# Performance work log

Hardware: AMD Instinct MI355X
Metric: run time of the kernel (lower is better)

Reference implementation:

```python
import jax, jax.numpy as jnp
import numpy as np

MAX_GRAD = 200.0


@jax.custom_vjp
def sqrt_bound_derivative(x):
    return jnp.sqrt(x)


def _sqrt_bd_fwd(x):
    return jnp.sqrt(x), x


def _sqrt_bd_bwd(x, g):
    # derivative of sqrt clipped to MAX_GRAD: 0.5/sqrt(x) <= MAX_GRAD  <=>  x >= 1/(4*MAX_GRAD^2)
    x_clipped = jnp.maximum(x, 1.0 / (4.0 * MAX_GRAD * MAX_GRAD))
    return (g * 0.5 / jnp.sqrt(x_clipped),)


sqrt_bound_derivative.defvjp(_sqrt_bd_fwd, _sqrt_bd_bwd)


def linear_scan(a, x, h0):
    # h_t = a_t * h_{t-1} + x_t, diagonal recurrence over axis=1 (time).
    # Parallel form via associative scan on pairs (a, b): combine -> (a1*a2, a2*b1 + b2).
    def combine(c1, c2):
        a1, b1 = c1
        a2, b2 = c2
        return a1 * a2, a2 * b1 + b2

    a_cum, h = jax.lax.associative_scan(combine, (a, x), axis=1)
    # fold in initial state: h_t += (prod_{u<=t} a_u) * h0
    h = h + a_cum * h0[:, None, :]
    return h, h[:, -1]


def setup_inputs() -> dict:
    key = jax.random.key(0)
    ks = jax.random.split(key, 8)
    B, S, D_IN, D_HID, D_OUT = 8, 4096, 512, 1024, 512
    R_MIN, R_MAX = 0.9, 0.999

    x = jax.random.normal(ks[0], (B, S, D_IN), dtype=jnp.float32)
    h0 = jnp.zeros((B, D_HID), dtype=jnp.float32)

    # stable_init: a_logit = logit(U(r_min, r_max)) so that a = sigmoid(a_logit) in [r_min, r_max]
    u = jax.random.uniform(ks[1], (D_HID,), minval=R_MIN, maxval=R_MAX)
    a_logit = jnp.log(u) - jnp.log1p(-u)

    def dense_init(k, d_in, d_out):
        scale = 1.0 / np.sqrt(d_in)
        return jax.random.uniform(k, (d_in, d_out), minval=-scale, maxval=scale).astype(jnp.float32)

    W_dx = dense_init(ks[2], D_IN, D_OUT)
    b_dx = jnp.zeros((D_OUT,), dtype=jnp.float32)
    W_in = dense_init(ks[3], D_IN, D_HID)
    b_in = jnp.zeros((D_HID,), dtype=jnp.float32)
    W_out = dense_init(ks[4], D_HID, D_OUT)
    b_out = jnp.zeros((D_OUT,), dtype=jnp.float32)

    return {"x": x, "h0": h0, "a_logit": a_logit,
            "W_dx": W_dx, "b_dx": b_dx,
            "W_in": W_in, "b_in": b_in,
            "W_out": W_out, "b_out": b_out}


def reference(x, h0, a_logit, W_dx, b_dx, W_in, b_in, W_out, b_out):
    a = jax.nn.sigmoid(a_logit)                      # (d_hidden,)
    dx = jnp.einsum('bsi,io->bso', x, W_dx) + b_dx   # skip projection (b, s, d_out)
    u = jnp.einsum('bsi,ih->bsh', x, W_in) + b_in    # input projection (b, s, d_hidden)
    u = sqrt_bound_derivative(1.0 - a * a) * u       # input_norm gating
    a_b = jnp.broadcast_to(a, u.shape)
    h, h_last = linear_scan(a_b, u, h0)              # diagonal linear recurrence
    out = (dx + jnp.einsum('bsh,ho->bso', h, W_out) + b_out) / 2.0
    return out, h_last
```

## Files before the change

### kernel.cpp

```cpp
#include <hip/hip_runtime.h>

#define B_    8
#define S_    4096
#define DIN   512
#define DHID  1024
#define DOUT  512
#define M_    (B_*S_)
#define NCAT  (DHID + DOUT)
#define CH2   32
#define NCH2  (S_/CH2)

typedef __bf16 bf16x8 __attribute__((ext_vector_type(8)));
typedef float  floatx4 __attribute__((ext_vector_type(4)));

__device__ __forceinline__ unsigned short f2bf(float f) {
  unsigned u = __builtin_bit_cast(unsigned, f);
  u = (u + 0x7FFFu + ((u >> 16) & 1u)) >> 16;
  return (unsigned short)u;
}
__device__ __forceinline__ float bf2f(unsigned short h) {
  unsigned u = ((unsigned)h) << 16;
  return __builtin_bit_cast(float, u);
}

__device__ __forceinline__ void gl_lds16(const unsigned short* g, unsigned short* l) {
  __builtin_amdgcn_global_load_lds((const __attribute__((address_space(1))) void*)g,
                                   (__attribute__((address_space(3))) void*)l, 16, 0, 0);
}

__global__ void prep_as(const float* __restrict__ logit, float* __restrict__ a_s) {
  int d = blockIdx.x * 256 + threadIdx.x;
  if (d < DHID) {
    float a = 1.f / (1.f + expf(-logit[d]));
    a_s[d] = a;
    a_s[DHID + d] = sqrtf(fmaxf(1.f - a * a, 0.f));
  }
}

__global__ void prep_x(const float* __restrict__ x, unsigned short* __restrict__ xb) {
  size_t i = (size_t)blockIdx.x * 256 + threadIdx.x;
  const float4* p = (const float4*)x;
  float4 v0 = p[i * 2];
  float4 v1 = p[i * 2 + 1];
  uint4 o;
  o.x = (unsigned)f2bf(v0.x) | ((unsigned)f2bf(v0.y) << 16);
  o.y = (unsigned)f2bf(v0.z) | ((unsigned)f2bf(v0.w) << 16);
  o.z = (unsigned)f2bf(v1.x) | ((unsigned)f2bf(v1.y) << 16);
  o.w = (unsigned)f2bf(v1.z) | ((unsigned)f2bf(v1.w) << 16);
  *(uint4*)&xb[i * 8] = o;
}

__global__ void prep_wcat(const float* __restrict__ Win, const float* __restrict__ Wdx,
                          unsigned short* __restrict__ wcat) {
  int idx = blockIdx.x * 256 + threadIdx.x;
  int n = idx >> 9, k = idx & 511;
  float v = (n < DHID) ? Win[(size_t)k * DHID + n] : Wdx[(size_t)k * DOUT + (n - DHID)];
  wcat[idx] = f2bf(v);
}

__global__ void prep_wout(const float* __restrict__ Wout, unsigned short* __restrict__ wt) {
  int idx = blockIdx.x * 256 + threadIdx.x;
  int n = idx >> 10, k = idx & 1023;
  wt[idx] = f2bf(Wout[(size_t)k * DOUT + n]);
}

template <int K, int MODE, int NB>
__global__ __launch_bounds__(256, 4) void gemm_bt(
    const unsigned short* __restrict__ A,
    const unsigned short* __restrict__ Bt,
    const float* __restrict__ a_s,
    const float* __restrict__ bias0,
    const float* __restrict__ bias1,
    unsigned short* __restrict__ u_out,
    unsigned short* __restrict__ dx_buf,
    float* __restrict__ out)
{
  __shared__ __align__(16) unsigned char smem[32768];
  unsigned short* lA = (unsigned short*)smem;
  unsigned short* lB = (unsigned short*)(smem + 16384);
  float* stg = (float*)smem;

  const int tid = threadIdx.x;
  const int flat = blockIdx.y * gridDim.x + blockIdx.x;
  const int xcd = flat & 7;
  const int j = flat >> 3;
  const int n0 = (j % NB) * 128;
  const int m0 = ((j / NB) * 8 + xcd) * 128;

  const int wid = tid >> 6, lane = tid & 63;
  const int wm = (wid >> 1) * 64, wn = (wid & 1) * 64;
  const int r16 = lane & 15, quad = lane >> 4;
  const int sw = r16 & 7;

  const int rsub = lane >> 3;
  const int gcol = ((lane & 7) ^ rsub) << 3;

  const unsigned short* Abase = A + (size_t)(m0 + (wid << 5) + rsub) * K + gcol;
  const unsigned short* Bbase = Bt + (size_t)(n0 + (wid << 5) + rsub) * K + gcol;
  unsigned short* lAw = lA + (wid << 5) * 64;
  unsigned short* lBw = lB + (wid << 5) * 64;

  floatx4 acc[4][4] = {};

  for (int k0 = 0; k0 < K; k0 += 64) {
#pragma unroll
    for (int i = 0; i < 4; ++i) {
      gl_lds16(Abase + (size_t)(i * 8) * K + k0, lAw + i * 8 * 64);
      gl_lds16(Bbase + (size_t)(i * 8) * K + k0, lBw + i * 8 * 64);
    }
    __syncthreads();
#pragma unroll
    for (int ks = 0; ks < 2; ++ks) {
      bf16x8 af[4], bfr[4];
#pragma unroll
      for (int i = 0; i < 4; ++i)
        af[i] = *(const bf16x8*)&lA[(wm + i * 16 + r16) * 64 + ((((ks << 2) | quad) ^ sw) << 3)];
#pragma unroll
      for (int j2 = 0; j2 < 4; ++j2)
        bfr[j2] = *(const bf16x8*)&lB[(wn + j2 * 16 + r16) * 64 + ((((ks << 2) | quad) ^ sw) << 3)];
#pragma unroll
      for (int i = 0; i < 4; ++i)
#pragma unroll
        for (int j2 = 0; j2 < 4; ++j2)
          acc[i][j2] = __builtin_amdgcn_mfma_f32_16x16x32_bf16(af[i], bfr[j2], acc[i][j2], 0, 0, 0);
    }
    __syncthreads();
  }

  const int row = tid >> 3;
  const int seg = tid & 7;
#pragma unroll
  for (int p = 0; p < 4; ++p) {
    __syncthreads();
    if ((wid >> 1) == (p >> 1)) {
      const int i0 = (p & 1) * 2;
#pragma unroll
      for (int ii = 0; ii < 2; ++ii) {
        const int i = i0 + ii;
        const int srow = i * 16 + quad * 4 - (p & 1) * 32;
#pragma unroll
        for (int j2 = 0; j2 < 4; ++j2) {
          const int scol = wn + j2 * 16 + r16;
#pragma unroll
          for (int r = 0; r < 4; ++r)
            stg[(srow + r) * 132 + scol] = acc[i][j2][r];
        }
      }
    }
    __syncthreads();
    const int gm = m0 + p * 32 + row;
    const int col0 = n0 + seg * 16;
    if (MODE == 0) {
      union { unsigned short s[16]; uint4 q[2]; } ub;
      if (n0 < DHID) {
#pragma unroll
        for (int u = 0; u < 4; ++u) {
          float4 v  = *(const float4*)&stg[row * 132 + seg * 16 + u * 4];
          float4 bi = *(const float4*)&bias0[col0 + u * 4];
          float4 sc = *(const float4*)&a_s[DHID + col0 + u * 4];
          ub.s[u * 4 + 0] = f2bf((v.x + bi.x) * sc.x);
          ub.s[u * 4 + 1] = f2bf((v.y + bi.y) * sc.y);
          ub.s[u * 4 + 2] = f2bf((v.z + bi.z) * sc.z);
          ub.s[u * 4 + 3] = f2bf((v.w + bi.w) * sc.w);
        }
        *(uint4*)&u_out[(size_t)gm * DHID + col0]     = ub.q[0];
        *(uint4*)&u_out[(size_t)gm * DHID + col0 + 8] = ub.q[1];
      } else {
        const int c2 = col0 - DHID;
#pragma unroll
        for (int u = 0; u < 4; ++u) {
          float4 v  = *(const float4*)&stg[row * 132 + seg * 16 + u * 4];
          float4 bd = *(const float4*)&bias1[c2 + u * 4];
          ub.s[u * 4 + 0] = f2bf(v.x + bd.x);
          ub.s[u * 4 + 1] = f2bf(v.y + bd.y);
          ub.s[u * 4 + 2] = f2bf(v.z + bd.z);
          ub.s[u * 4 + 3] = f2bf(v.w + bd.w);
        }
        *(uint4*)&dx_buf[(size_t)gm * DOUT + c2]     = ub.q[0];
        *(uint4*)&dx_buf[(size_t)gm * DOUT + c2 + 8] = ub.q[1];
      }
    } else {
#pragma unroll
      for (int u = 0; u < 4; ++u) {
        float4 v  = *(const float4*)&stg[row * 132 + seg * 16 + u * 4];
        float4 bo = *(const float4*)&bias0[col0 + u * 4];
        ushort4 dv = *(const ushort4*)&dx_buf[(size_t)gm * DOUT + col0 + u * 4];
        float4 o;
        o.x = (v.x + bo.x + bf2f(dv.x)) * 0.5f;
        o.y = (v.y + bo.y + bf2f(dv.y)) * 0.5f;
        o.z = (v.z + bo.z + bf2f(dv.z)) * 0.5f;
        o.w = (v.w + bo.w + bf2f(dv.w)) * 0.5f;
        *(float4*)&out[(size_t)gm * DOUT + col0 + u * 4] = o;
      }
    }
  }
}

__global__ __launch_bounds__(256) void scan1(const unsigned short* __restrict__ u,
                                             const float* __restrict__ a_s,
                                             float* __restrict__ carry) {
  int idx = blockIdx.x * 256 + threadIdx.x;
  int d8 = (idx & 127) * 8;
  int c  = (idx >> 7) & (NCH2 - 1);
  int b  = idx >> 14;
  float4 a0 = *(const float4*)&a_s[d8];
  float4 a1 = *(const float4*)&a_s[d8 + 4];
  float h0_ = 0.f, h1 = 0.f, h2 = 0.f, h3 = 0.f, h4 = 0.f, h5 = 0.f, h6 = 0.f, h7 = 0.f;
  const unsigned short* up = u + ((size_t)(b * S_ + c * CH2)) * DHID + d8;
#pragma unroll 4
  for (int t = 0; t < CH2; ++t) {
    ushort4 q0 = *(const ushort4*)up;
    ushort4 q1 = *(const ushort4*)(up + 4);
    h0_ = fmaf(a0.x, h0_, bf2f(q0.x)); h1 = fmaf(a0.y, h1, bf2f(q0.y));
    h2  = fmaf(a0.z, h2,  bf2f(q0.z)); h3 = fmaf(a0.w, h3, bf2f(q0.w));
    h4  = fmaf(a1.x, h4,  bf2f(q1.x)); h5 = fmaf(a1.y, h5, bf2f(q1.y));
    h6  = fmaf(a1.z, h6,  bf2f(q1.z)); h7 = fmaf(a1.w, h7, bf2f(q1.w));
    up += DHID;
  }
  float* cp = &carry[((size_t)(b * NCH2 + c)) * DHID + d8];
  float4 o0 = {h0_, h1, h2, h3}, o1 = {h4, h5, h6, h7};
  *(float4*)cp = o0;
  *(float4*)(cp + 4) = o1;
}

__global__ __launch_bounds__(256) void scan_mid(const float* __restrict__ a_s,
                                                const float* __restrict__ h0,
                                                float* __restrict__ carry,
                                                float* __restrict__ h_last) {
  int idx = blockIdx.x * 256 + threadIdx.x;
  int d = idx & (DHID - 1);
  int b = idx >> 10;
  float a = a_s[d];
  float aL = a;
#pragma unroll
  for (int q = 0; q < 5; ++q) aL *= aL;
  float st = h0[(size_t)b * DHID + d];
  float* p = &carry[(size_t)b * NCH2 * DHID + d];
  for (int cg = 0; cg < NCH2; cg += 8) {
    float loc[8];
#pragma unroll
    for (int j = 0; j < 8; ++j) loc[j] = p[(size_t)j * DHID];
#pragma unroll
    for (int j = 0; j < 8; ++j) {
      p[(size_t)j * DHID] = st;
      st = fmaf(aL, st, loc[j]);
    }
    p += (size_t)8 * DHID;
  }
  h_last[(size_t)b * DHID + d] = st;
}

__global__ __launch_bounds__(256) void scan2(unsigned short* __restrict__ u,
                                             const float* __restrict__ a_s,
                                             const float* __restrict__ carry) {
  int idx = blockIdx.x * 256 + threadIdx.x;
  int d8 = (idx & 127) * 8;
  int c  = (idx >> 7) & (NCH2 - 1);
  int b  = idx >> 14;
  float4 a0 = *(const float4*)&a_s[d8];
  float4 a1 = *(const float4*)&a_s[d8 + 4];
  const float* cp = &carry[((size_t)(b * NCH2 + c)) * DHID + d8];
  float4 e0 = *(const float4*)cp;
  float4 e1 = *(const float4*)(cp + 4);
  float h0_ = e0.x, h1 = e0.y, h2 = e0.z, h3 = e0.w;
  float h4 = e1.x, h5 = e1.y, h6 = e1.z, h7 = e1.w;
  unsigned short* up = u + ((size_t)(b * S_ + c * CH2)) * DHID + d8;
#pragma unroll 4
  for (int t = 0; t < CH2; ++t) {
    ushort4 q0 = *(const ushort4*)up;
    ushort4 q1 = *(const ushort4*)(up + 4);
    h0_ = fmaf(a0.x, h0_, bf2f(q0.x)); h1 = fmaf(a0.y, h1, bf2f(q0.y));
    h2  = fmaf(a0.z, h2,  bf2f(q0.z)); h3 = fmaf(a0.w, h3, bf2f(q0.w));
    h4  = fmaf(a1.x, h4,  bf2f(q1.x)); h5 = fmaf(a1.y, h5, bf2f(q1.y));
    h6  = fmaf(a1.z, h6,  bf2f(q1.z)); h7 = fmaf(a1.w, h7, bf2f(q1.w));
    ushort4 w0, w1;
    w0.x = f2bf(h0_); w0.y = f2bf(h1); w0.z = f2bf(h2); w0.w = f2bf(h3);
    w1.x = f2bf(h4);  w1.y = f2bf(h5); w1.z = f2bf(h6); w1.w = f2bf(h7);
    *(ushort4*)up = w0;
    *(ushort4*)(up + 4) = w1;
    up += DHID;
  }
}

extern "C" void kernel_launch(void* const* d_in, const int* in_sizes, int n_in,
                              void* d_out, int out_size, void* d_ws, size_t ws_size,
                              hipStream_t stream) {
  const float* x    = (const float*)d_in[0];
  const float* h0   = (const float*)d_in[1];
  const float* alog = (const float*)d_in[2];
  const float* Wdx  = (const float*)d_in[3];
  const float* bdx  = (const float*)d_in[4];
  const float* Win  = (const float*)d_in[5];
  const float* bin  = (const float*)d_in[6];
  const float* Wout = (const float*)d_in[7];
  const float* bout = (const float*)d_in[8];

  float* out    = (float*)d_out;
  float* h_last = out + (size_t)M_ * DOUT;

  char* ws = (char*)d_ws;
  unsigned short* xb    = (unsigned short*)(ws);
  unsigned short* ubuf  = (unsigned short*)(ws + 33554432ull);
  unsigned short* dxb   = (unsigned short*)(ws + 100663296ull);
  unsigned short* wcat  = (unsigned short*)(ws + 134217728ull);
  unsigned short* woutt = (unsigned short*)(ws + 135790592ull);
  float*          a_s   = (float*)(ws + 136839168ull);
  float*          carry = (float*)(ws);

  prep_as  <<<4, 256, 0, stream>>>(alog, a_s);
  prep_x   <<<(M_ * DIN / 8) / 256, 256, 0, stream>>>(x, xb);
  prep_wcat<<<(NCAT * DIN) / 256, 256, 0, stream>>>(Win, Wdx, wcat);
  prep_wout<<<(DOUT * DHID) / 256, 256, 0, stream>>>(Wout, woutt);

  gemm_bt<DIN, 0, 12><<<dim3(NCAT / 128, M_ / 128), 256, 0, stream>>>(
      xb, wcat, a_s, bin, bdx, ubuf, dxb, nullptr);

  scan1   <<<(B_ * NCH2 * (DHID / 8)) / 256, 256, 0, stream>>>(ubuf, a_s, carry);
  scan_mid<<<(B_ * DHID) / 256, 256, 0, stream>>>(a_s, h0, carry, h_last);
  scan2   <<<(B_ * NCH2 * (DHID / 8)) / 256, 256, 0, stream>>>(ubuf, a_s, carry);

  gemm_bt<DHID, 1, 4><<<dim3(DOUT / 128, M_ / 128), 256, 0, stream>>>(
      ubuf, woutt, a_s, bout, nullptr, nullptr, dxb, out);
}
```

Baseline: 296.3 us.

## Fuse fp32-to-bf16 conversion of x into GEMM A-tile loads, merge prep kernels

The first GEMM now reads x directly in fp32 and converts to bf16 in registers before writing the A tile to LDS. This removes the separate prep_x pass and its bf16 copy in the workspace. A-tile loads move from async global-to-LDS into registers and are prefetched one K-step ahead. The three weight and parameter prep kernels are merged into one launch, and launch bounds drop from 4 to 3 waves per SIMD. The trade-off is twice the global read bytes for A in the first GEMM, which is re-read by 12 N-blocks, plus higher register pressure.

```diff
diff --git a/kernel.cpp b/kernel.cpp
--- a/kernel.cpp
+++ b/kernel.cpp
@@ -28,45 +28,36 @@
                                    (__attribute__((address_space(3))) void*)l, 16, 0, 0);
 }
 
-__global__ void prep_as(const float* __restrict__ logit, float* __restrict__ a_s) {
-  int d = blockIdx.x * 256 + threadIdx.x;
-  if (d < DHID) {
-    float a = 1.f / (1.f + expf(-logit[d]));
-    a_s[d] = a;
-    a_s[DHID + d] = sqrtf(fmaxf(1.f - a * a, 0.f));
-  }
-}
-
-__global__ void prep_x(const float* __restrict__ x, unsigned short* __restrict__ xb) {
-  size_t i = (size_t)blockIdx.x * 256 + threadIdx.x;
-  const float4* p = (const float4*)x;
-  float4 v0 = p[i * 2];
-  float4 v1 = p[i * 2 + 1];
-  uint4 o;
-  o.x = (unsigned)f2bf(v0.x) | ((unsigned)f2bf(v0.y) << 16);
-  o.y = (unsigned)f2bf(v0.z) | ((unsigned)f2bf(v0.w) << 16);
-  o.z = (unsigned)f2bf(v1.x) | ((unsigned)f2bf(v1.y) << 16);
-  o.w = (unsigned)f2bf(v1.z) | ((unsigned)f2bf(v1.w) << 16);
-  *(uint4*)&xb[i * 8] = o;
-}
-
-__global__ void prep_wcat(const float* __restrict__ Win, const float* __restrict__ Wdx,
-                          unsigned short* __restrict__ wcat) {
-  int idx = blockIdx.x * 256 + threadIdx.x;
-  int n = idx >> 9, k = idx & 511;
-  float v = (n < DHID) ? Win[(size_t)k * DHID + n] : Wdx[(size_t)k * DOUT + (n - DHID)];
-  wcat[idx] = f2bf(v);
-}
-
-__global__ void prep_wout(const float* __restrict__ Wout, unsigned short* __restrict__ wt) {
-  int idx = blockIdx.x * 256 + threadIdx.x;
-  int n = idx >> 10, k = idx & 1023;
-  wt[idx] = f2bf(Wout[(size_t)k * DOUT + n]);
+__global__ void prep_all(const float* __restrict__ logit,
+                         const float* __restrict__ Win, const float* __restrict__ Wdx,
+                         const float* __restrict__ Wout,
+                         float* __restrict__ a_s,
+                         unsigned short* __restrict__ wcat,
+                         unsigned short* __restrict__ woutt) {
+  int bx = blockIdx.x;
+  if (bx < 3072) {
+    int idx = bx * 256 + threadIdx.x;
+    int n = idx >> 9, k = idx & 511;
+    float v = (n < DHID) ? Win[(size_t)k * DHID + n] : Wdx[(size_t)k * DOUT + (n - DHID)];
+    wcat[idx] = f2bf(v);
+  } else if (bx < 5120) {
+    int idx = (bx - 3072) * 256 + threadIdx.x;
+    int n = idx >> 10, k = idx & 1023;
+    woutt[idx] = f2bf(Wout[(size_t)k * DOUT + n]);
+  } else {
+    int d = (bx - 5120) * 256 + threadIdx.x;
+    if (d < DHID) {
+      float a = 1.f / (1.f + expf(-logit[d]));
+      a_s[d] = a;
+      a_s[DHID + d] = sqrtf(fmaxf(1.f - a * a, 0.f));
+    }
+  }
 }
 
 template <int K, int MODE, int NB>
-__global__ __launch_bounds__(256, 4) void gemm_bt(
-    const unsigned short* __restrict__ A,
+__global__ __launch_bounds__(256, 3) void gemm_bt(
+    const float* __restrict__ Af,
+    const unsigned short* __restrict__ Ab,
     const unsigned short* __restrict__ Bt,
     const float* __restrict__ a_s,
     const float* __restrict__ bias0,
@@ -95,20 +86,41 @@
   const int rsub = lane >> 3;
   const int gcol = ((lane & 7) ^ rsub) << 3;
 
-  const unsigned short* Abase = A + (size_t)(m0 + (wid << 5) + rsub) * K + gcol;
-  const unsigned short* Bbase = Bt + (size_t)(n0 + (wid << 5) + rsub) * K + gcol;
-  unsigned short* lAw = lA + (wid << 5) * 64;
+  const int arow = (wid << 5) + rsub;
+  const unsigned short* Bbase = Bt + (size_t)(n0 + arow) * K + gcol;
   unsigned short* lBw = lB + (wid << 5) * 64;
+  unsigned short* lAst = lA + ((wid << 5) + rsub) * 64 + (lane & 7) * 8;
 
   floatx4 acc[4][4] = {};
-
+  bf16x8 apre[4];
+
+  auto loadA = [&](int k0) {
+#pragma unroll
+    for (int i = 0; i < 4; ++i) {
+      if (MODE == 0) {
+        const float* src = Af + (size_t)(m0 + arow + i * 8) * K + k0 + gcol;
+        float4 f0 = *(const float4*)src;
+        float4 f1 = *(const float4*)(src + 4);
+        union { unsigned short s[8]; bf16x8 v; } t;
+        t.s[0] = f2bf(f0.x); t.s[1] = f2bf(f0.y); t.s[2] = f2bf(f0.z); t.s[3] = f2bf(f0.w);
+        t.s[4] = f2bf(f1.x); t.s[5] = f2bf(f1.y); t.s[6] = f2bf(f1.z); t.s[7] = f2bf(f1.w);
+        apre[i] = t.v;
+      } else {
+        apre[i] = *(const bf16x8*)(Ab + (size_t)(m0 + arow + i * 8) * K + k0 + gcol);
+      }
+    }
+  };
+
+  loadA(0);
   for (int k0 = 0; k0 < K; k0 += 64) {
 #pragma unroll
-    for (int i = 0; i < 4; ++i) {
-      gl_lds16(Abase + (size_t)(i * 8) * K + k0, lAw + i * 8 * 64);
+    for (int i = 0; i < 4; ++i)
+      *(bf16x8*)(lAst + i * 8 * 64) = apre[i];
+#pragma unroll
+    for (int i = 0; i < 4; ++i)
       gl_lds16(Bbase + (size_t)(i * 8) * K + k0, lBw + i * 8 * 64);
-    }
     __syncthreads();
+    if (k0 + 64 < K) loadA(k0 + 64);
 #pragma unroll
     for (int ks = 0; ks < 2; ++ks) {
       bf16x8 af[4], bfr[4];
@@ -299,26 +311,22 @@
   float* h_last = out + (size_t)M_ * DOUT;
 
   char* ws = (char*)d_ws;
-  unsigned short* xb    = (unsigned short*)(ws);
-  unsigned short* ubuf  = (unsigned short*)(ws + 33554432ull);
-  unsigned short* dxb   = (unsigned short*)(ws + 100663296ull);
-  unsigned short* wcat  = (unsigned short*)(ws + 134217728ull);
-  unsigned short* woutt = (unsigned short*)(ws + 135790592ull);
-  float*          a_s   = (float*)(ws + 136839168ull);
-  float*          carry = (float*)(ws);
-
-  prep_as  <<<4, 256, 0, stream>>>(alog, a_s);
-  prep_x   <<<(M_ * DIN / 8) / 256, 256, 0, stream>>>(x, xb);
-  prep_wcat<<<(NCAT * DIN) / 256, 256, 0, stream>>>(Win, Wdx, wcat);
-  prep_wout<<<(DOUT * DHID) / 256, 256, 0, stream>>>(Wout, woutt);
+  unsigned short* ubuf  = (unsigned short*)(ws);
+  unsigned short* dxb   = (unsigned short*)(ws + 67108864ull);
+  unsigned short* wcat  = (unsigned short*)(ws + 100663296ull);
+  unsigned short* woutt = (unsigned short*)(ws + 102236160ull);
+  float*          a_s   = (float*)(ws + 103284736ull);
+  float*          carry = (float*)(ws + 103292928ull);
+
+  prep_all<<<5124, 256, 0, stream>>>(alog, Win, Wdx, Wout, a_s, wcat, woutt);
 
   gemm_bt<DIN, 0, 12><<<dim3(NCAT / 128, M_ / 128), 256, 0, stream>>>(
-      xb, wcat, a_s, bin, bdx, ubuf, dxb, nullptr);
+      x, nullptr, wcat, a_s, bin, bdx, ubuf, dxb, nullptr);
 
   scan1   <<<(B_ * NCH2 * (DHID / 8)) / 256, 256, 0, stream>>>(ubuf, a_s, carry);
   scan_mid<<<(B_ * DHID) / 256, 256, 0, stream>>>(a_s, h0, carry, h_last);
   scan2   <<<(B_ * NCH2 * (DHID / 8)) / 256, 256, 0, stream>>>(ubuf, a_s, carry);
 
   gemm_bt<DHID, 1, 4><<<dim3(DOUT / 128, M_ / 128), 256, 0, stream>>>(
-      ubuf, woutt, a_s, bout, nullptr, nullptr, dxb, out);
-}
+      nullptr, ubuf, woutt, a_s, bout, nullptr, nullptr, dxb, out);
+}
```

After: 347.2 us. 17.2% more time.

## Fuse chunk-carry scan into first GEMM epilogue and merge prep kernels

Applied to the files above, without the earlier changes.

The first-pass chunk scan (scan1) is folded into the input-projection GEMM epilogue. Each 32-row chunk's local recurrence carry is computed from the fp32 staged tile in LDS and written directly, so the separate pass that re-read the whole bf16 u buffer is gone. The four prep kernels are merged into one launch to cut launch overhead. The epilogue gains an extra sync and serial 16-step FMA chains per p-iteration, and the carry buffer moves to its own workspace region, no longer aliasing the xb scratch.

```diff
diff --git a/kernel.cpp b/kernel.cpp
--- a/kernel.cpp
+++ b/kernel.cpp
@@ -28,40 +28,42 @@
                                    (__attribute__((address_space(3))) void*)l, 16, 0, 0);
 }
 
-__global__ void prep_as(const float* __restrict__ logit, float* __restrict__ a_s) {
-  int d = blockIdx.x * 256 + threadIdx.x;
-  if (d < DHID) {
-    float a = 1.f / (1.f + expf(-logit[d]));
-    a_s[d] = a;
-    a_s[DHID + d] = sqrtf(fmaxf(1.f - a * a, 0.f));
-  }
-}
-
-__global__ void prep_x(const float* __restrict__ x, unsigned short* __restrict__ xb) {
-  size_t i = (size_t)blockIdx.x * 256 + threadIdx.x;
-  const float4* p = (const float4*)x;
-  float4 v0 = p[i * 2];
-  float4 v1 = p[i * 2 + 1];
-  uint4 o;
-  o.x = (unsigned)f2bf(v0.x) | ((unsigned)f2bf(v0.y) << 16);
-  o.y = (unsigned)f2bf(v0.z) | ((unsigned)f2bf(v0.w) << 16);
-  o.z = (unsigned)f2bf(v1.x) | ((unsigned)f2bf(v1.y) << 16);
-  o.w = (unsigned)f2bf(v1.z) | ((unsigned)f2bf(v1.w) << 16);
-  *(uint4*)&xb[i * 8] = o;
-}
-
-__global__ void prep_wcat(const float* __restrict__ Win, const float* __restrict__ Wdx,
-                          unsigned short* __restrict__ wcat) {
-  int idx = blockIdx.x * 256 + threadIdx.x;
-  int n = idx >> 9, k = idx & 511;
-  float v = (n < DHID) ? Win[(size_t)k * DHID + n] : Wdx[(size_t)k * DOUT + (n - DHID)];
-  wcat[idx] = f2bf(v);
-}
-
-__global__ void prep_wout(const float* __restrict__ Wout, unsigned short* __restrict__ wt) {
-  int idx = blockIdx.x * 256 + threadIdx.x;
-  int n = idx >> 10, k = idx & 1023;
-  wt[idx] = f2bf(Wout[(size_t)k * DOUT + n]);
+__global__ void prep_all(const float* __restrict__ logit,
+                         const float* __restrict__ Win, const float* __restrict__ Wdx,
+                         const float* __restrict__ Wout, const float* __restrict__ x,
+                         float* __restrict__ a_s,
+                         unsigned short* __restrict__ wcat,
+                         unsigned short* __restrict__ woutt,
+                         unsigned short* __restrict__ xb) {
+  int bx = blockIdx.x;
+  if (bx < 3072) {
+    int idx = bx * 256 + threadIdx.x;
+    int n = idx >> 9, k = idx & 511;
+    float v = (n < DHID) ? Win[(size_t)k * DHID + n] : Wdx[(size_t)k * DOUT + (n - DHID)];
+    wcat[idx] = f2bf(v);
+  } else if (bx < 5120) {
+    int idx = (bx - 3072) * 256 + threadIdx.x;
+    int n = idx >> 10, k = idx & 1023;
+    woutt[idx] = f2bf(Wout[(size_t)k * DOUT + n]);
+  } else if (bx < 5124) {
+    int d = (bx - 5120) * 256 + threadIdx.x;
+    if (d < DHID) {
+      float a = 1.f / (1.f + expf(-logit[d]));
+      a_s[d] = a;
+      a_s[DHID + d] = sqrtf(fmaxf(1.f - a * a, 0.f));
+    }
+  } else {
+    size_t i = (size_t)(bx - 5124) * 256 + threadIdx.x;
+    const float4* p = (const float4*)x;
+    float4 v0 = p[i * 2];
+    float4 v1 = p[i * 2 + 1];
+    uint4 o;
+    o.x = (unsigned)f2bf(v0.x) | ((unsigned)f2bf(v0.y) << 16);
+    o.y = (unsigned)f2bf(v0.z) | ((unsigned)f2bf(v0.w) << 16);
+    o.z = (unsigned)f2bf(v1.x) | ((unsigned)f2bf(v1.y) << 16);
+    o.w = (unsigned)f2bf(v1.z) | ((unsigned)f2bf(v1.w) << 16);
+    *(uint4*)&xb[i * 8] = o;
+  }
 }
 
 template <int K, int MODE, int NB>
@@ -73,12 +75,14 @@
     const float* __restrict__ bias1,
     unsigned short* __restrict__ u_out,
     unsigned short* __restrict__ dx_buf,
-    float* __restrict__ out)
+    float* __restrict__ out,
+    float* __restrict__ carry)
 {
   __shared__ __align__(16) unsigned char smem[32768];
   unsigned short* lA = (unsigned short*)smem;
   unsigned short* lB = (unsigned short*)(smem + 16384);
-  float* stg = (float*)smem;
+  float* stg  = (float*)smem;
+  float* ltmp = (float*)(smem + 16896);
 
   const int tid = threadIdx.x;
   const int flat = blockIdx.y * gridDim.x + blockIdx.x;
@@ -129,6 +133,19 @@
 
   const int row = tid >> 3;
   const int seg = tid & 7;
+  const int scol_ = tid & 127;
+  const int shalf = tid >> 7;
+  float aa = 0.f, sbi = 0.f, ssc = 0.f, a16 = 0.f;
+  if (MODE == 0 && n0 < DHID) {
+    aa  = a_s[n0 + scol_];
+    sbi = bias0[n0 + scol_];
+    ssc = a_s[DHID + n0 + scol_];
+    float t2 = aa * aa, t4 = t2 * t2, t8 = t4 * t4;
+    a16 = t8 * t8;
+  }
+  const int bb = m0 >> 12;
+  const int c0 = (m0 & 4095) >> 5;
+
 #pragma unroll
   for (int p = 0; p < 4; ++p) {
     __syncthreads();
@@ -148,6 +165,21 @@
       }
     }
     __syncthreads();
+
+    if (MODE == 0 && n0 < DHID) {
+      float P = 0.f;
+      const float* sp = &stg[(shalf * 16) * 132 + scol_];
+#pragma unroll
+      for (int r = 0; r < 16; ++r) {
+        P = fmaf(aa, P, (sp[0] + sbi) * ssc);
+        sp += 132;
+      }
+      if (shalf) ltmp[scol_] = P;
+      __syncthreads();
+      if (!shalf)
+        carry[((size_t)bb * NCH2 + c0 + p) * DHID + n0 + scol_] = fmaf(a16, P, ltmp[scol_]);
+    }
+
     const int gm = m0 + p * 32 + row;
     const int col0 = n0 + seg * 16;
     if (MODE == 0) {
@@ -194,33 +226,6 @@
       }
     }
   }
-}
-
-__global__ __launch_bounds__(256) void scan1(const unsigned short* __restrict__ u,
-                                             const float* __restrict__ a_s,
-                                             float* __restrict__ carry) {
-  int idx = blockIdx.x * 256 + threadIdx.x;
-  int d8 = (idx & 127) * 8;
-  int c  = (idx >> 7) & (NCH2 - 1);
-  int b  = idx >> 14;
-  float4 a0 = *(const float4*)&a_s[d8];
-  float4 a1 = *(const float4*)&a_s[d8 + 4];
-  float h0_ = 0.f, h1 = 0.f, h2 = 0.f, h3 = 0.f, h4 = 0.f, h5 = 0.f, h6 = 0.f, h7 = 0.f;
-  const unsigned short* up = u + ((size_t)(b * S_ + c * CH2)) * DHID + d8;
-#pragma unroll 4
-  for (int t = 0; t < CH2; ++t) {
-    ushort4 q0 = *(const ushort4*)up;
-    ushort4 q1 = *(const ushort4*)(up + 4);
-    h0_ = fmaf(a0.x, h0_, bf2f(q0.x)); h1 = fmaf(a0.y, h1, bf2f(q0.y));
-    h2  = fmaf(a0.z, h2,  bf2f(q0.z)); h3 = fmaf(a0.w, h3, bf2f(q0.w));
-    h4  = fmaf(a1.x, h4,  bf2f(q1.x)); h5 = fmaf(a1.y, h5, bf2f(q1.y));
-    h6  = fmaf(a1.z, h6,  bf2f(q1.z)); h7 = fmaf(a1.w, h7, bf2f(q1.w));
-    up += DHID;
-  }
-  float* cp = &carry[((size_t)(b * NCH2 + c)) * DHID + d8];
-  float4 o0 = {h0_, h1, h2, h3}, o1 = {h4, h5, h6, h7};
-  *(float4*)cp = o0;
-  *(float4*)(cp + 4) = o1;
 }
 
 __global__ __launch_bounds__(256) void scan_mid(const float* __restrict__ a_s,
@@ -305,20 +310,17 @@
   unsigned short* wcat  = (unsigned short*)(ws + 134217728ull);
   unsigned short* woutt = (unsigned short*)(ws + 135790592ull);
   float*          a_s   = (float*)(ws + 136839168ull);
-  float*          carry = (float*)(ws);
-
-  prep_as  <<<4, 256, 0, stream>>>(alog, a_s);
-  prep_x   <<<(M_ * DIN / 8) / 256, 256, 0, stream>>>(x, xb);
-  prep_wcat<<<(NCAT * DIN) / 256, 256, 0, stream>>>(Win, Wdx, wcat);
-  prep_wout<<<(DOUT * DHID) / 256, 256, 0, stream>>>(Wout, woutt);
+  float*          carry = (float*)(ws + 136847360ull);
+
+  prep_all<<<5124 + (M_ * DIN / 8) / 256, 256, 0, stream>>>(
+      alog, Win, Wdx, Wout, x, a_s, wcat, woutt, xb);
 
   gemm_bt<DIN, 0, 12><<<dim3(NCAT / 128, M_ / 128), 256, 0, stream>>>(
-      xb, wcat, a_s, bin, bdx, ubuf, dxb, nullptr);
-
-  scan1   <<<(B_ * NCH2 * (DHID / 8)) / 256, 256, 0, stream>>>(ubuf, a_s, carry);
+      xb, wcat, a_s, bin, bdx, ubuf, dxb, nullptr, carry);
+
   scan_mid<<<(B_ * DHID) / 256, 256, 0, stream>>>(a_s, h0, carry, h_last);
   scan2   <<<(B_ * NCH2 * (DHID / 8)) / 256, 256, 0, stream>>>(ubuf, a_s, carry);
 
   gemm_bt<DHID, 1, 4><<<dim3(DOUT / 128, M_ / 128), 256, 0, stream>>>(
-      ubuf, woutt, a_s, bout, nullptr, nullptr, dxb, out);
-}
+      ubuf, woutt, a_s, bout, nullptr, nullptr, dxb, out, nullptr);
+}
```

Measured after the change: 293.7 us. Within noise of the previous version (-0.9%).
